# Performance work log

Measured on AMD Instinct MI355X. Metric: run time of the kernel, lower is better.

## Reference

```python
import jax, jax.numpy as jnp
import numpy as np

USER_VOCAB = 1_000_000
MOVIE_VOCAB = 100_000
EMB_DIM = 64
BATCH = 65536
H1, H2 = 256, 128  # over_arch_layer_sizes


def setup_inputs() -> dict:
    key = jax.random.key(0)
    ks = jax.random.split(key, 10)
    inv = 1.0 / np.sqrt(EMB_DIM)
    return {
        "user_ids": jax.random.randint(ks[0], (BATCH,), 0, USER_VOCAB),
        "movie_ids": jax.random.randint(ks[1], (BATCH,), 0, MOVIE_VOCAB),
        "emb_user": jax.random.normal(ks[2], (USER_VOCAB, EMB_DIM), jnp.float32) * inv,
        "emb_movie": jax.random.normal(ks[3], (MOVIE_VOCAB, EMB_DIM), jnp.float32) * inv,
        "W1": jax.random.normal(ks[4], (EMB_DIM, H1), jnp.float32) * (1.0 / np.sqrt(EMB_DIM)),
        "b1": jnp.zeros((H1,), jnp.float32),
        "W2": jax.random.normal(ks[5], (H1, H2), jnp.float32) * (1.0 / np.sqrt(H1)),
        "b2": jnp.zeros((H2,), jnp.float32),
        "W3": jax.random.normal(ks[6], (H2, 1), jnp.float32) * (1.0 / np.sqrt(H2)),
        "b3": jnp.zeros((1,), jnp.float32),
    }


def reference(user_ids, movie_ids, emb_user, emb_movie, W1, b1, W2, b2, W3, b3):
    B = user_ids.shape[0]
    # sparse gather per feature (hotness = 1)
    eu = emb_user[user_ids]    # [B, D]
    em = emb_movie[movie_ids]  # [B, D]
    # concat jagged outputs along rows, matching torch.cat(..., dim=0)
    x = jnp.concatenate([eu, em], axis=0)  # [2B, D]
    h = jax.nn.relu(x @ W1 + b1)
    h = jax.nn.relu(h @ W2 + b2)
    p = h @ W3 + b3                        # [2B, 1]
    # view(num_features, batch).t().sum(-1) -> sum over features per sample
    return p.reshape(2, B).sum(axis=0)     # [B]
```

## Files before the change

kernel.cpp:

```cpp
#include <hip/hip_runtime.h>


typedef __attribute__((ext_vector_type(8))) short bf16x8;
typedef __attribute__((ext_vector_type(16))) float f32x16;

__device__ __forceinline__ unsigned int cvt_pk(float lo, float hi) {
  unsigned int r;
  asm("v_cvt_pk_bf16_f32 %0, %1, %2" : "=v"(r) : "v"(lo), "v"(hi));
  return r;
}

__global__ __launch_bounds__(512, 2) void movielens_mlp(
    const int* __restrict__ uids, const int* __restrict__ mids,
    const float* __restrict__ EU, const float* __restrict__ EM,
    const float* __restrict__ W1, const float* __restrict__ B1,
    const float* __restrict__ W2, const float* __restrict__ B2,
    const float* __restrict__ W3, const float* __restrict__ B3,
    float* __restrict__ out) {
  __shared__ __align__(16) unsigned short w1f[32 * 512];
  __shared__ __align__(16) unsigned short w2f[64 * 512];

  const int tid = threadIdx.x;
  const int lane = tid & 63, wv = tid >> 6;
  const int m32 = lane & 31, H = lane >> 5;

  const int sbase = blockIdx.x * 256 + wv * 32;
  const int sid = sbase + m32;

  const float* rowU = EU + (size_t)uids[sid] * 64;
  const float* rowM = EM + (size_t)mids[sid] * 64;
  float4 xr[2][4][2];
#pragma unroll
  for (int kk = 0; kk < 4; ++kk) {
    xr[0][kk][0] = *(const float4*)(rowU + 16 * kk + 8 * H);
    xr[0][kk][1] = *(const float4*)(rowU + 16 * kk + 8 * H + 4);
    xr[1][kk][0] = *(const float4*)(rowM + 16 * kk + 8 * H);
    xr[1][kk][1] = *(const float4*)(rowM + 16 * kk + 8 * H + 4);
  }

#pragma unroll
  for (int i = 0; i < 6; ++i) {
    const int u = tid + 512 * i;
    const int cq = u & 7, bb = (u >> 3) & 1, hh = (u >> 4) & 1;
    if (i < 2) {
      const int fi = u >> 5;
      const int ct = fi >> 2, kk = fi & 3;
      const float* src = W1 + (16 * kk + 8 * hh + 4 * bb) * 256 + 32 * ct + 4 * cq;
      const float4 r0 = *(const float4*)(src);
      const float4 r1 = *(const float4*)(src + 256);
      const float4 r2 = *(const float4*)(src + 512);
      const float4 r3 = *(const float4*)(src + 768);
      const float c0[4] = {r0.x, r0.y, r0.z, r0.w};
      const float c1[4] = {r1.x, r1.y, r1.z, r1.w};
      const float c2[4] = {r2.x, r2.y, r2.z, r2.w};
      const float c3[4] = {r3.x, r3.y, r3.z, r3.w};
      const int slot0 = 32 * hh + 16 * (cq >> 2) + 8 * (cq & 1) + 4 * ((cq >> 1) & 1);
#pragma unroll
      for (int s = 0; s < 4; ++s) {
        uint2 pk;
        pk.x = cvt_pk(c0[s], c1[s]);
        pk.y = cvt_pk(c2[s], c3[s]);
        *(uint2*)&w1f[fi * 512 + (slot0 + s) * 8 + 4 * bb] = pk;
      }
    } else {
      const int v = u - 1024;
      const int f2 = v >> 5;
      const int ks = f2 >> 2, n2 = f2 & 3;
      const float* src = W2 + (16 * ks + 8 * hh + 4 * bb) * 128 + 32 * n2 + 4 * cq;
      const float4 r0 = *(const float4*)(src);
      const float4 r1 = *(const float4*)(src + 128);
      const float4 r2 = *(const float4*)(src + 256);
      const float4 r3 = *(const float4*)(src + 384);
      const float c0[4] = {r0.x, r0.y, r0.z, r0.w};
      const float c1[4] = {r1.x, r1.y, r1.z, r1.w};
      const float c2[4] = {r2.x, r2.y, r2.z, r2.w};
      const float c3[4] = {r3.x, r3.y, r3.z, r3.w};
      const int slot0 = 32 * hh + 4 * cq;
#pragma unroll
      for (int s = 0; s < 4; ++s) {
        uint2 pk;
        pk.x = cvt_pk(c0[s], c1[s]);
        pk.y = cvt_pk(c2[s], c3[s]);
        *(uint2*)&w2f[f2 * 512 + (slot0 + s) * 8 + 4 * bb] = pk;
      }
    }
  }

  bf16x8 xf[2][4];
#pragma unroll
  for (int t = 0; t < 2; ++t)
#pragma unroll
    for (int kk = 0; kk < 4; ++kk) {
      const float4 a = xr[t][kk][0], b = xr[t][kk][1];
      uint4 w;
      w.x = cvt_pk(a.x, a.y);
      w.y = cvt_pk(a.z, a.w);
      w.z = cvt_pk(b.x, b.y);
      w.w = cvt_pk(b.z, b.w);
      xf[t][kk] = __builtin_bit_cast(bf16x8, w);
    }
  __syncthreads();

  f32x16 acc2[2][4];
#pragma unroll
  for (int n2 = 0; n2 < 4; ++n2)
#pragma unroll
    for (int rq = 0; rq < 4; ++rq) {
      const float4 bq = *(const float4*)(B2 + 32 * n2 + 8 * rq + 4 * H);
      const float bv[4] = {bq.x, bq.y, bq.z, bq.w};
#pragma unroll
      for (int s = 0; s < 4; ++s) {
        acc2[0][n2][4 * rq + s] = bv[s];
        acc2[1][n2][4 * rq + s] = bv[s];
      }
    }

  bf16x8 a1[4];
#pragma unroll
  for (int kk = 0; kk < 4; ++kk)
    a1[kk] = *(const bf16x8*)&w1f[kk * 512 + lane * 8];

#pragma unroll 2
  for (int ct = 0; ct < 8; ++ct) {
    f32x16 acc1a;
    {
      const float4 q0 = *(const float4*)(B1 + 32 * ct + 8 * H);
      const float4 q1 = *(const float4*)(B1 + 32 * ct + 8 * H + 4);
      const float4 q2 = *(const float4*)(B1 + 32 * ct + 8 * H + 16);
      const float4 q3 = *(const float4*)(B1 + 32 * ct + 8 * H + 20);
      acc1a[0]=q0.x; acc1a[1]=q0.y; acc1a[2]=q0.z; acc1a[3]=q0.w;
      acc1a[4]=q1.x; acc1a[5]=q1.y; acc1a[6]=q1.z; acc1a[7]=q1.w;
      acc1a[8]=q2.x; acc1a[9]=q2.y; acc1a[10]=q2.z; acc1a[11]=q2.w;
      acc1a[12]=q3.x; acc1a[13]=q3.y; acc1a[14]=q3.z; acc1a[15]=q3.w;
    }
#pragma unroll
    for (int kk = 0; kk < 4; ++kk)
      acc1a = __builtin_amdgcn_mfma_f32_32x32x16_bf16(a1[kk], xf[0][kk], acc1a, 0, 0, 0);

    bf16x8 w2v[8];
#pragma unroll
    for (int q = 0; q < 8; ++q)
      w2v[q] = *(const bf16x8*)&w2f[(8 * ct + q) * 512 + lane * 8];

    uint4 lo0, hi0;
    lo0.x = cvt_pk(fmaxf(acc1a[0], 0.f), fmaxf(acc1a[1], 0.f));
    lo0.y = cvt_pk(fmaxf(acc1a[2], 0.f), fmaxf(acc1a[3], 0.f));
    lo0.z = cvt_pk(fmaxf(acc1a[4], 0.f), fmaxf(acc1a[5], 0.f));
    lo0.w = cvt_pk(fmaxf(acc1a[6], 0.f), fmaxf(acc1a[7], 0.f));
    hi0.x = cvt_pk(fmaxf(acc1a[8], 0.f), fmaxf(acc1a[9], 0.f));
    hi0.y = cvt_pk(fmaxf(acc1a[10], 0.f), fmaxf(acc1a[11], 0.f));
    hi0.z = cvt_pk(fmaxf(acc1a[12], 0.f), fmaxf(acc1a[13], 0.f));
    hi0.w = cvt_pk(fmaxf(acc1a[14], 0.f), fmaxf(acc1a[15], 0.f));

    f32x16 acc1b;
    {
      const float4 q0 = *(const float4*)(B1 + 32 * ct + 8 * H);
      const float4 q1 = *(const float4*)(B1 + 32 * ct + 8 * H + 4);
      const float4 q2 = *(const float4*)(B1 + 32 * ct + 8 * H + 16);
      const float4 q3 = *(const float4*)(B1 + 32 * ct + 8 * H + 20);
      acc1b[0]=q0.x; acc1b[1]=q0.y; acc1b[2]=q0.z; acc1b[3]=q0.w;
      acc1b[4]=q1.x; acc1b[5]=q1.y; acc1b[6]=q1.z; acc1b[7]=q1.w;
      acc1b[8]=q2.x; acc1b[9]=q2.y; acc1b[10]=q2.z; acc1b[11]=q2.w;
      acc1b[12]=q3.x; acc1b[13]=q3.y; acc1b[14]=q3.z; acc1b[15]=q3.w;
    }
#pragma unroll
    for (int kk = 0; kk < 4; ++kk)
      acc1b = __builtin_amdgcn_mfma_f32_32x32x16_bf16(a1[kk], xf[1][kk], acc1b, 0, 0, 0);

    if (ct < 7) {
#pragma unroll
      for (int kk = 0; kk < 4; ++kk)
        a1[kk] = *(const bf16x8*)&w1f[((ct + 1) * 4 + kk) * 512 + lane * 8];
    }

#pragma unroll
    for (int n2 = 0; n2 < 4; ++n2) {
      acc2[0][n2] = __builtin_amdgcn_mfma_f32_32x32x16_bf16(
          w2v[n2], __builtin_bit_cast(bf16x8, lo0), acc2[0][n2], 0, 0, 0);
      acc2[0][n2] = __builtin_amdgcn_mfma_f32_32x32x16_bf16(
          w2v[4 + n2], __builtin_bit_cast(bf16x8, hi0), acc2[0][n2], 0, 0, 0);
    }

    uint4 lo1, hi1;
    lo1.x = cvt_pk(fmaxf(acc1b[0], 0.f), fmaxf(acc1b[1], 0.f));
    lo1.y = cvt_pk(fmaxf(acc1b[2], 0.f), fmaxf(acc1b[3], 0.f));
    lo1.z = cvt_pk(fmaxf(acc1b[4], 0.f), fmaxf(acc1b[5], 0.f));
    lo1.w = cvt_pk(fmaxf(acc1b[6], 0.f), fmaxf(acc1b[7], 0.f));
    hi1.x = cvt_pk(fmaxf(acc1b[8], 0.f), fmaxf(acc1b[9], 0.f));
    hi1.y = cvt_pk(fmaxf(acc1b[10], 0.f), fmaxf(acc1b[11], 0.f));
    hi1.z = cvt_pk(fmaxf(acc1b[12], 0.f), fmaxf(acc1b[13], 0.f));
    hi1.w = cvt_pk(fmaxf(acc1b[14], 0.f), fmaxf(acc1b[15], 0.f));

#pragma unroll
    for (int n2 = 0; n2 < 4; ++n2) {
      acc2[1][n2] = __builtin_amdgcn_mfma_f32_32x32x16_bf16(
          w2v[n2], __builtin_bit_cast(bf16x8, lo1), acc2[1][n2], 0, 0, 0);
      acc2[1][n2] = __builtin_amdgcn_mfma_f32_32x32x16_bf16(
          w2v[4 + n2], __builtin_bit_cast(bf16x8, hi1), acc2[1][n2], 0, 0, 0);
    }
  }

  float part = 0.f;
#pragma unroll
  for (int n2 = 0; n2 < 4; ++n2) {
#pragma unroll
    for (int rq = 0; rq < 4; ++rq) {
      const float4 wq = *(const float4*)(W3 + 32 * n2 + 8 * rq + 4 * H);
      const float wv4[4] = {wq.x, wq.y, wq.z, wq.w};
#pragma unroll
      for (int s = 0; s < 4; ++s) {
        part += fmaxf(acc2[0][n2][4 * rq + s], 0.f) * wv4[s];
        part += fmaxf(acc2[1][n2][4 * rq + s], 0.f) * wv4[s];
      }
    }
  }
  part += __shfl_xor(part, 32, 64);
  if (lane < 32) out[sbase + lane] = part + 2.f * B3[0];
}

extern "C" void kernel_launch(void* const* d_in, const int* in_sizes, int n_in,
                              void* d_out, int out_size, void* d_ws, size_t ws_size,
                              hipStream_t stream) {
  const int* uids = (const int*)d_in[0];
  const int* mids = (const int*)d_in[1];
  const float* EU = (const float*)d_in[2];
  const float* EM = (const float*)d_in[3];
  const float* W1 = (const float*)d_in[4];
  const float* B1 = (const float*)d_in[5];
  const float* W2 = (const float*)d_in[6];
  const float* B2 = (const float*)d_in[7];
  const float* W3 = (const float*)d_in[8];
  const float* B3 = (const float*)d_in[9];
  float* out = (float*)d_out;

  const int B = in_sizes[0];
  const int nblk = B / 256;
  hipLaunchKernelGGL(movielens_mlp, dim3(nblk), dim3(512), 0, stream,
                     uids, mids, EU, EM, W1, B1, W2, B2, W3, B3, out);
}
```

Before: 21.79 us.

## Stream W2 staging into LDS in passes overlapped with layer-1/2 MFMA loop

Weight staging is restructured so W1 and only the first quarter of W2 are converted to bf16 and written to LDS before the first barrier. The remaining W2 quarters are loaded into registers and written during early iterations of the compute loop, with extra barriers. The aim is to shorten the prologue before MFMA work begins. The change also fully unrolls the ct loop, shares the bias init between both feature halves, interleaves the layer-2 MFMAs with per-use LDS loads, and uses nontemporal loads for embedding rows and the output store. Risks include higher register pressure from full unrolling and held W2 registers, plus the extra barrier stalls.

```diff
diff --git a/kernel.cpp b/kernel.cpp
--- a/kernel.cpp
+++ b/kernel.cpp
@@ -3,6 +3,7 @@
 
 typedef __attribute__((ext_vector_type(8))) short bf16x8;
 typedef __attribute__((ext_vector_type(16))) float f32x16;
+typedef __attribute__((ext_vector_type(4))) float f32x4n;
 
 __device__ __forceinline__ unsigned int cvt_pk(float lo, float hi) {
   unsigned int r;
@@ -23,75 +24,89 @@
   const int tid = threadIdx.x;
   const int lane = tid & 63, wv = tid >> 6;
   const int m32 = lane & 31, H = lane >> 5;
-
   const int sbase = blockIdx.x * 256 + wv * 32;
   const int sid = sbase + m32;
 
-  const float* rowU = EU + (size_t)uids[sid] * 64;
-  const float* rowM = EM + (size_t)mids[sid] * 64;
-  float4 xr[2][4][2];
+  const int uid = uids[sid];
+  const int mid = mids[sid];
+
+  const int cq = tid & 7, bb = (tid >> 3) & 1, hh = (tid >> 4) & 1;
+
+  float4 w1r[2][4];
+#pragma unroll
+  for (int i = 0; i < 2; ++i) {
+    const int fi = (tid >> 5) + 16 * i;
+    const int ct = fi >> 2, kk = fi & 3;
+    const float* s = W1 + (16 * kk + 8 * hh + 4 * bb) * 256 + 32 * ct + 4 * cq;
+    w1r[i][0] = *(const float4*)(s);
+    w1r[i][1] = *(const float4*)(s + 256);
+    w1r[i][2] = *(const float4*)(s + 512);
+    w1r[i][3] = *(const float4*)(s + 768);
+  }
+  float4 w2r[2][4];
+  auto w2_load = [&](int pass, float4 r[4]) {
+    const int f2 = (tid >> 5) + 16 * pass;
+    const int ks = f2 >> 2, n2 = f2 & 3;
+    const float* s = W2 + (16 * ks + 8 * hh + 4 * bb) * 128 + 32 * n2 + 4 * cq;
+    r[0] = *(const float4*)(s);
+    r[1] = *(const float4*)(s + 128);
+    r[2] = *(const float4*)(s + 256);
+    r[3] = *(const float4*)(s + 384);
+  };
+  w2_load(0, w2r[0]);
+  w2_load(1, w2r[1]);
+
+  const float* rowU = EU + (size_t)uid * 64;
+  const float* rowM = EM + (size_t)mid * 64;
+  f32x4n xr[2][4][2];
 #pragma unroll
   for (int kk = 0; kk < 4; ++kk) {
-    xr[0][kk][0] = *(const float4*)(rowU + 16 * kk + 8 * H);
-    xr[0][kk][1] = *(const float4*)(rowU + 16 * kk + 8 * H + 4);
-    xr[1][kk][0] = *(const float4*)(rowM + 16 * kk + 8 * H);
-    xr[1][kk][1] = *(const float4*)(rowM + 16 * kk + 8 * H + 4);
-  }
-
-#pragma unroll
-  for (int i = 0; i < 6; ++i) {
-    const int u = tid + 512 * i;
-    const int cq = u & 7, bb = (u >> 3) & 1, hh = (u >> 4) & 1;
-    if (i < 2) {
-      const int fi = u >> 5;
-      const int ct = fi >> 2, kk = fi & 3;
-      const float* src = W1 + (16 * kk + 8 * hh + 4 * bb) * 256 + 32 * ct + 4 * cq;
-      const float4 r0 = *(const float4*)(src);
-      const float4 r1 = *(const float4*)(src + 256);
-      const float4 r2 = *(const float4*)(src + 512);
-      const float4 r3 = *(const float4*)(src + 768);
-      const float c0[4] = {r0.x, r0.y, r0.z, r0.w};
-      const float c1[4] = {r1.x, r1.y, r1.z, r1.w};
-      const float c2[4] = {r2.x, r2.y, r2.z, r2.w};
-      const float c3[4] = {r3.x, r3.y, r3.z, r3.w};
-      const int slot0 = 32 * hh + 16 * (cq >> 2) + 8 * (cq & 1) + 4 * ((cq >> 1) & 1);
-#pragma unroll
-      for (int s = 0; s < 4; ++s) {
-        uint2 pk;
-        pk.x = cvt_pk(c0[s], c1[s]);
-        pk.y = cvt_pk(c2[s], c3[s]);
-        *(uint2*)&w1f[fi * 512 + (slot0 + s) * 8 + 4 * bb] = pk;
-      }
-    } else {
-      const int v = u - 1024;
-      const int f2 = v >> 5;
-      const int ks = f2 >> 2, n2 = f2 & 3;
-      const float* src = W2 + (16 * ks + 8 * hh + 4 * bb) * 128 + 32 * n2 + 4 * cq;
-      const float4 r0 = *(const float4*)(src);
-      const float4 r1 = *(const float4*)(src + 128);
-      const float4 r2 = *(const float4*)(src + 256);
-      const float4 r3 = *(const float4*)(src + 384);
-      const float c0[4] = {r0.x, r0.y, r0.z, r0.w};
-      const float c1[4] = {r1.x, r1.y, r1.z, r1.w};
-      const float c2[4] = {r2.x, r2.y, r2.z, r2.w};
-      const float c3[4] = {r3.x, r3.y, r3.z, r3.w};
-      const int slot0 = 32 * hh + 4 * cq;
-#pragma unroll
-      for (int s = 0; s < 4; ++s) {
-        uint2 pk;
-        pk.x = cvt_pk(c0[s], c1[s]);
-        pk.y = cvt_pk(c2[s], c3[s]);
-        *(uint2*)&w2f[f2 * 512 + (slot0 + s) * 8 + 4 * bb] = pk;
-      }
-    }
-  }
+    xr[0][kk][0] = __builtin_nontemporal_load((const f32x4n*)(rowU + 16 * kk + 8 * H));
+    xr[0][kk][1] = __builtin_nontemporal_load((const f32x4n*)(rowU + 16 * kk + 8 * H + 4));
+    xr[1][kk][0] = __builtin_nontemporal_load((const f32x4n*)(rowM + 16 * kk + 8 * H));
+    xr[1][kk][1] = __builtin_nontemporal_load((const f32x4n*)(rowM + 16 * kk + 8 * H + 4));
+  }
+
+  const int w1slot0 = 32 * hh + 16 * (cq >> 2) + 8 * (cq & 1) + 4 * ((cq >> 1) & 1);
+#pragma unroll
+  for (int i = 0; i < 2; ++i) {
+    const int fi = (tid >> 5) + 16 * i;
+    const float c0[4] = {w1r[i][0].x, w1r[i][0].y, w1r[i][0].z, w1r[i][0].w};
+    const float c1[4] = {w1r[i][1].x, w1r[i][1].y, w1r[i][1].z, w1r[i][1].w};
+    const float c2[4] = {w1r[i][2].x, w1r[i][2].y, w1r[i][2].z, w1r[i][2].w};
+    const float c3[4] = {w1r[i][3].x, w1r[i][3].y, w1r[i][3].z, w1r[i][3].w};
+#pragma unroll
+    for (int s = 0; s < 4; ++s) {
+      uint2 pk;
+      pk.x = cvt_pk(c0[s], c1[s]);
+      pk.y = cvt_pk(c2[s], c3[s]);
+      *(uint2*)&w1f[fi * 512 + (w1slot0 + s) * 8 + 4 * bb] = pk;
+    }
+  }
+  auto w2_write = [&](int pass, const float4 r[4]) {
+    const int f2 = (tid >> 5) + 16 * pass;
+    const int slot0 = 32 * hh + 4 * cq;
+    const float c0[4] = {r[0].x, r[0].y, r[0].z, r[0].w};
+    const float c1[4] = {r[1].x, r[1].y, r[1].z, r[1].w};
+    const float c2[4] = {r[2].x, r[2].y, r[2].z, r[2].w};
+    const float c3[4] = {r[3].x, r[3].y, r[3].z, r[3].w};
+#pragma unroll
+    for (int s = 0; s < 4; ++s) {
+      uint2 pk;
+      pk.x = cvt_pk(c0[s], c1[s]);
+      pk.y = cvt_pk(c2[s], c3[s]);
+      *(uint2*)&w2f[f2 * 512 + (slot0 + s) * 8 + 4 * bb] = pk;
+    }
+  };
+  w2_write(0, w2r[0]);
+  __syncthreads();
 
   bf16x8 xf[2][4];
 #pragma unroll
   for (int t = 0; t < 2; ++t)
 #pragma unroll
     for (int kk = 0; kk < 4; ++kk) {
-      const float4 a = xr[t][kk][0], b = xr[t][kk][1];
+      const f32x4n a = xr[t][kk][0], b = xr[t][kk][1];
       uint4 w;
       w.x = cvt_pk(a.x, a.y);
       w.y = cvt_pk(a.z, a.w);
@@ -99,7 +114,6 @@
       w.w = cvt_pk(b.z, b.w);
       xf[t][kk] = __builtin_bit_cast(bf16x8, w);
     }
-  __syncthreads();
 
   f32x16 acc2[2][4];
 #pragma unroll
@@ -120,28 +134,22 @@
   for (int kk = 0; kk < 4; ++kk)
     a1[kk] = *(const bf16x8*)&w1f[kk * 512 + lane * 8];
 
-#pragma unroll 2
+#pragma unroll
   for (int ct = 0; ct < 8; ++ct) {
-    f32x16 acc1a;
-    {
-      const float4 q0 = *(const float4*)(B1 + 32 * ct + 8 * H);
-      const float4 q1 = *(const float4*)(B1 + 32 * ct + 8 * H + 4);
-      const float4 q2 = *(const float4*)(B1 + 32 * ct + 8 * H + 16);
-      const float4 q3 = *(const float4*)(B1 + 32 * ct + 8 * H + 20);
-      acc1a[0]=q0.x; acc1a[1]=q0.y; acc1a[2]=q0.z; acc1a[3]=q0.w;
-      acc1a[4]=q1.x; acc1a[5]=q1.y; acc1a[6]=q1.z; acc1a[7]=q1.w;
-      acc1a[8]=q2.x; acc1a[9]=q2.y; acc1a[10]=q2.z; acc1a[11]=q2.w;
-      acc1a[12]=q3.x; acc1a[13]=q3.y; acc1a[14]=q3.z; acc1a[15]=q3.w;
-    }
+    const float4 q0 = *(const float4*)(B1 + 32 * ct + 8 * H);
+    const float4 q1 = *(const float4*)(B1 + 32 * ct + 8 * H + 4);
+    const float4 q2 = *(const float4*)(B1 + 32 * ct + 8 * H + 16);
+    const float4 q3 = *(const float4*)(B1 + 32 * ct + 8 * H + 20);
+    f32x16 binit;
+    binit[0] = q0.x; binit[1] = q0.y; binit[2] = q0.z; binit[3] = q0.w;
+    binit[4] = q1.x; binit[5] = q1.y; binit[6] = q1.z; binit[7] = q1.w;
+    binit[8] = q2.x; binit[9] = q2.y; binit[10] = q2.z; binit[11] = q2.w;
+    binit[12] = q3.x; binit[13] = q3.y; binit[14] = q3.z; binit[15] = q3.w;
+
+    f32x16 acc1a = binit;
 #pragma unroll
     for (int kk = 0; kk < 4; ++kk)
       acc1a = __builtin_amdgcn_mfma_f32_32x32x16_bf16(a1[kk], xf[0][kk], acc1a, 0, 0, 0);
-
-    bf16x8 w2v[8];
-#pragma unroll
-    for (int q = 0; q < 8; ++q)
-      w2v[q] = *(const bf16x8*)&w2f[(8 * ct + q) * 512 + lane * 8];
-
     uint4 lo0, hi0;
     lo0.x = cvt_pk(fmaxf(acc1a[0], 0.f), fmaxf(acc1a[1], 0.f));
     lo0.y = cvt_pk(fmaxf(acc1a[2], 0.f), fmaxf(acc1a[3], 0.f));
@@ -152,35 +160,10 @@
     hi0.z = cvt_pk(fmaxf(acc1a[12], 0.f), fmaxf(acc1a[13], 0.f));
     hi0.w = cvt_pk(fmaxf(acc1a[14], 0.f), fmaxf(acc1a[15], 0.f));
 
-    f32x16 acc1b;
-    {
-      const float4 q0 = *(const float4*)(B1 + 32 * ct + 8 * H);
-      const float4 q1 = *(const float4*)(B1 + 32 * ct + 8 * H + 4);
-      const float4 q2 = *(const float4*)(B1 + 32 * ct + 8 * H + 16);
-      const float4 q3 = *(const float4*)(B1 + 32 * ct + 8 * H + 20);
-      acc1b[0]=q0.x; acc1b[1]=q0.y; acc1b[2]=q0.z; acc1b[3]=q0.w;
-      acc1b[4]=q1.x; acc1b[5]=q1.y; acc1b[6]=q1.z; acc1b[7]=q1.w;
-      acc1b[8]=q2.x; acc1b[9]=q2.y; acc1b[10]=q2.z; acc1b[11]=q2.w;
-      acc1b[12]=q3.x; acc1b[13]=q3.y; acc1b[14]=q3.z; acc1b[15]=q3.w;
-    }
+    f32x16 acc1b = binit;
 #pragma unroll
     for (int kk = 0; kk < 4; ++kk)
       acc1b = __builtin_amdgcn_mfma_f32_32x32x16_bf16(a1[kk], xf[1][kk], acc1b, 0, 0, 0);
-
-    if (ct < 7) {
-#pragma unroll
-      for (int kk = 0; kk < 4; ++kk)
-        a1[kk] = *(const bf16x8*)&w1f[((ct + 1) * 4 + kk) * 512 + lane * 8];
-    }
-
-#pragma unroll
-    for (int n2 = 0; n2 < 4; ++n2) {
-      acc2[0][n2] = __builtin_amdgcn_mfma_f32_32x32x16_bf16(
-          w2v[n2], __builtin_bit_cast(bf16x8, lo0), acc2[0][n2], 0, 0, 0);
-      acc2[0][n2] = __builtin_amdgcn_mfma_f32_32x32x16_bf16(
-          w2v[4 + n2], __builtin_bit_cast(bf16x8, hi0), acc2[0][n2], 0, 0, 0);
-    }
-
     uint4 lo1, hi1;
     lo1.x = cvt_pk(fmaxf(acc1b[0], 0.f), fmaxf(acc1b[1], 0.f));
     lo1.y = cvt_pk(fmaxf(acc1b[2], 0.f), fmaxf(acc1b[3], 0.f));
@@ -191,12 +174,40 @@
     hi1.z = cvt_pk(fmaxf(acc1b[12], 0.f), fmaxf(acc1b[13], 0.f));
     hi1.w = cvt_pk(fmaxf(acc1b[14], 0.f), fmaxf(acc1b[15], 0.f));
 
-#pragma unroll
-    for (int n2 = 0; n2 < 4; ++n2) {
-      acc2[1][n2] = __builtin_amdgcn_mfma_f32_32x32x16_bf16(
-          w2v[n2], __builtin_bit_cast(bf16x8, lo1), acc2[1][n2], 0, 0, 0);
-      acc2[1][n2] = __builtin_amdgcn_mfma_f32_32x32x16_bf16(
-          w2v[4 + n2], __builtin_bit_cast(bf16x8, hi1), acc2[1][n2], 0, 0, 0);
+    if (ct < 7) {
+#pragma unroll
+      for (int kk = 0; kk < 4; ++kk)
+        a1[kk] = *(const bf16x8*)&w1f[((ct + 1) * 4 + kk) * 512 + lane * 8];
+    }
+
+#pragma unroll
+    for (int q = 0; q < 4; ++q) {
+      const bf16x8 wlo = *(const bf16x8*)&w2f[(8 * ct + q) * 512 + lane * 8];
+      acc2[0][q] = __builtin_amdgcn_mfma_f32_32x32x16_bf16(
+          wlo, __builtin_bit_cast(bf16x8, lo0), acc2[0][q], 0, 0, 0);
+      acc2[1][q] = __builtin_amdgcn_mfma_f32_32x32x16_bf16(
+          wlo, __builtin_bit_cast(bf16x8, lo1), acc2[1][q], 0, 0, 0);
+    }
+#pragma unroll
+    for (int q = 0; q < 4; ++q) {
+      const bf16x8 whi = *(const bf16x8*)&w2f[(8 * ct + 4 + q) * 512 + lane * 8];
+      acc2[0][q] = __builtin_amdgcn_mfma_f32_32x32x16_bf16(
+          whi, __builtin_bit_cast(bf16x8, hi0), acc2[0][q], 0, 0, 0);
+      acc2[1][q] = __builtin_amdgcn_mfma_f32_32x32x16_bf16(
+          whi, __builtin_bit_cast(bf16x8, hi1), acc2[1][q], 0, 0, 0);
+    }
+
+    if (ct == 0) {
+      w2_write(1, w2r[1]);
+      w2_load(2, w2r[0]);
+      __syncthreads();
+    } else if (ct == 2) {
+      w2_write(2, w2r[0]);
+      w2_load(3, w2r[1]);
+      __syncthreads();
+    } else if (ct == 4) {
+      w2_write(3, w2r[1]);
+      __syncthreads();
     }
   }
 
@@ -215,7 +226,9 @@
     }
   }
   part += __shfl_xor(part, 32, 64);
-  if (lane < 32) out[sbase + lane] = part + 2.f * B3[0];
+  if (lane < 32) {
+    __builtin_nontemporal_store(part + 2.f * B3[0], out + sbase + lane);
+  }
 }
 
 extern "C" void kernel_launch(void* const* d_in, const int* in_sizes, int n_in,
```

Result: slower. 26.49 us (+21.6%).
